# Kernel tuning notes

Hardware: AMD Instinct MI355X
Metric: run time of the kernel (lower is better)

Reference implementation:

```python
import jax, jax.numpy as jnp
import numpy as np

ALPHA = 0.1
BETA = 0.3
MARGIN = 2.0


def setup_inputs() -> dict:
    key = jax.random.key(0)
    k1, k2 = jax.random.split(key)
    prediction = jax.random.normal(k1, (8, 2048, 512), dtype=jnp.float32)
    target_seg = jax.random.randint(k2, (8, 2048), 0, 16, dtype=jnp.int64)
    return {"prediction": prediction, "target_seg": target_seg}


def _pairwise_sqdist(x):
    # x: [n, L, d] -> squared Euclidean distances [n, L, L] via a GEMM
    sq = jnp.sum(x * x, axis=-1)  # [n, L]
    inner = jnp.einsum('nld,nmd->nlm', x, x)  # [n, L, L]
    d2 = sq[:, :, None] + sq[:, None, :] - 2.0 * inner
    return jnp.maximum(d2, 0.0)


def _safe_sqrt(d2):
    # sqrt with zero (not NaN) gradient at 0, matching torch.cdist behavior
    pos = d2 > 0
    return jnp.where(pos, jnp.sqrt(jnp.where(pos, d2, 1.0)), 0.0)


def reference(prediction, target_seg):
    # y[i,j,k] = 1 if target_seg[i,j] == target_seg[i,k]
    y = (target_seg[:, :, None] == target_seg[:, None, :]).astype(prediction.dtype)
    d2 = _pairwise_sqdist(prediction)
    dist = _safe_sqrt(d2)
    hinge = jnp.maximum(MARGIN - dist, 0.0)
    loss = ALPHA * y * d2 + BETA * (1.0 - y) * hinge * hinge
    return jnp.mean(loss)
```

## Files before the change

kernel.cpp:

```cpp
#include <hip/hip_runtime.h>
#include <hip/hip_fp8.h>
#include <math.h>

#define L      2048
#define DDIM   512
#define NBATCH 8
#define NTJ    16
#define TOTAL_BLOCKS (NBATCH * NTJ * 4)

#define PANSZ  16384

#define ALPHA  0.1f
#define BETA   0.3f
#define MARGIN 2.0f

typedef __attribute__((ext_vector_type(16))) float f32x16;
typedef long long2v __attribute__((ext_vector_type(2)));

#define GLOAD_LDS16(g, l) __builtin_amdgcn_global_load_lds(              \
    (const __attribute__((address_space(1))) unsigned int*)(g),          \
    (__attribute__((address_space(3))) unsigned int*)(l), 16, 0, 0)

__global__ __launch_bounds__(256) void conv_kernel(const float* __restrict__ pred,
                                                   unsigned char* __restrict__ h,
                                                   float* __restrict__ sq) {
    int w     = threadIdx.x >> 6;
    int lane  = threadIdx.x & 63;
    int batch = blockIdx.x & 7;
    int idx   = blockIdx.x >> 3;
    int row   = batch * L + idx * 4 + w;
    const float* p = pred + (size_t)row * DDIM + lane * 8;
    float4 v0 = *(const float4*)(p);
    float4 v1 = *(const float4*)(p + 4);
    float vals[8] = {v0.x, v0.y, v0.z, v0.w, v1.x, v1.y, v1.z, v1.w};
    unsigned q[8];
    float s = 0.0f;
    #pragma unroll
    for (int i = 0; i < 8; ++i) {
        float x = vals[i];
        s = fmaf(x, x, s);
        __hip_fp8_e4m3 f8(x);
        q[i] = (unsigned)f8.__x;
    }
    unsigned lo = q[0] | (q[1] << 8) | (q[2] << 16) | (q[3] << 24);
    unsigned hi = q[4] | (q[5] << 8) | (q[6] << 16) | (q[7] << 24);
    int r5    = row & 31;
    int pair  = lane >> 2;
    int khalf = lane & 1;
    int kodd  = (lane >> 1) & 1;
    size_t off = (size_t)(row >> 5) * PANSZ + pair * 1024
               + (r5 + 32 * khalf) * 16 + kodd * 8;
    *(uint2*)(h + off) = make_uint2(lo, hi);
    #pragma unroll
    for (int o = 32; o > 0; o >>= 1) s += __shfl_down(s, o);
    if (lane == 0) sq[row] = s;
}

__global__ __launch_bounds__(256, 2) void loss_kernel(
        const unsigned char* __restrict__ h,
        const int*   __restrict__ seg,
        const float* __restrict__ sq,
        double*      __restrict__ partials) {
    __shared__ unsigned char As[65536];

    int bid = blockIdx.x;
    int n   = bid & 7;
    int r   = bid >> 3;
    int tj  = r >> 2;
    int q4  = r & 3;

    int t    = threadIdx.x;
    int wid  = t >> 6;
    int lane = t & 63;
    int wr   = wid >> 1;
    int wn   = wid & 1;
    int l31  = lane & 31;
    int hsel = lane >> 5;

    const unsigned char* base = h + (size_t)n * L * DDIM;

    {
        const unsigned char* asrc = base + (size_t)(tj * 4 + wid) * PANSZ + lane * 16;
        unsigned char* adst = As + wid * PANSZ;
        #pragma unroll
        for (int i = 0; i < 16; ++i)
            GLOAD_LDS16(asrc + i * 1024, adst + i * 1024);
    }
    __syncthreads();

    const int*   segb = seg + n * L;
    const float* sqb  = sq + n * L;

    float lsum = 0.0f;
    int aoff0 = (wr * 2 + 0) * PANSZ + lane * 16;
    int aoff1 = (wr * 2 + 1) * PANSZ + lane * 16;

    #pragma unroll 1
    for (int tkx = 0; tkx < 4; ++tkx) {
        int tk = q4 * 4 + tkx;
        const unsigned char* pb0 = base + (size_t)(tk * 4 + wn * 2) * PANSZ + lane * 16;
        const unsigned char* pb1 = pb0 + PANSZ;

        f32x16 acc[2][2];
        #pragma unroll
        for (int m = 0; m < 2; ++m)
            #pragma unroll
            for (int nf = 0; nf < 2; ++nf)
                #pragma unroll
                for (int x = 0; x < 16; ++x) acc[m][nf][x] = 0.0f;

        #pragma unroll
        for (int ks2 = 0; ks2 < 16; ++ks2) {
            long2v a0 = *(const long2v*)&As[aoff0 + ks2 * 1024];
            long2v a1 = *(const long2v*)&As[aoff1 + ks2 * 1024];
            long2v b0 = *(const long2v*)(pb0 + ks2 * 1024);
            long2v b1 = *(const long2v*)(pb1 + ks2 * 1024);
            acc[0][0] = __builtin_amdgcn_mfma_f32_32x32x16_fp8_fp8(a0.x, b0.x, acc[0][0], 0, 0, 0);
            acc[0][1] = __builtin_amdgcn_mfma_f32_32x32x16_fp8_fp8(a0.x, b1.x, acc[0][1], 0, 0, 0);
            acc[1][0] = __builtin_amdgcn_mfma_f32_32x32x16_fp8_fp8(a1.x, b0.x, acc[1][0], 0, 0, 0);
            acc[1][1] = __builtin_amdgcn_mfma_f32_32x32x16_fp8_fp8(a1.x, b1.x, acc[1][1], 0, 0, 0);
            acc[0][0] = __builtin_amdgcn_mfma_f32_32x32x16_fp8_fp8(a0.y, b0.y, acc[0][0], 0, 0, 0);
            acc[0][1] = __builtin_amdgcn_mfma_f32_32x32x16_fp8_fp8(a0.y, b1.y, acc[0][1], 0, 0, 0);
            acc[1][0] = __builtin_amdgcn_mfma_f32_32x32x16_fp8_fp8(a1.y, b0.y, acc[1][0], 0, 0, 0);
            acc[1][1] = __builtin_amdgcn_mfma_f32_32x32x16_fp8_fp8(a1.y, b1.y, acc[1][1], 0, 0, 0);
        }

        #pragma unroll
        for (int nf = 0; nf < 2; ++nf) {
            int k = tk * 128 + wn * 64 + nf * 32 + l31;
            float sqk = sqb[k];
            int   sgk = segb[k];
            #pragma unroll
            for (int m = 0; m < 2; ++m)
                #pragma unroll
                for (int x = 0; x < 16; ++x) {
                    int j = tj * 128 + wr * 64 + m * 32
                          + (x & 3) + 8 * (x >> 2) + 4 * hsel;
                    float inner = acc[m][nf][x];
                    float d2 = fmaxf(sqb[j] + sqk - 2.0f * inner, 0.0f);
                    float v;
                    if (segb[j] == sgk) {
                        v = ALPHA * d2;
                    } else {
                        float dist = sqrtf(d2);
                        float hg = fmaxf(MARGIN - dist, 0.0f);
                        v = BETA * hg * hg;
                    }
                    lsum += v;
                }
        }
    }

    double dsum = (double)lsum;
    #pragma unroll
    for (int off = 32; off > 0; off >>= 1)
        dsum += __shfl_down(dsum, off);
    if (lane == 0) partials[bid * 4 + wid] = dsum;
}

__global__ __launch_bounds__(256) void reduce_kernel(const double* __restrict__ partials,
                                                     float* __restrict__ out,
                                                     int nPart, double invCount) {
    __shared__ double red[256];
    int t = threadIdx.x;
    double s = 0.0;
    for (int i = t; i < nPart; i += 256) s += partials[i];
    red[t] = s;
    __syncthreads();
    #pragma unroll
    for (int k = 128; k > 0; k >>= 1) {
        if (t < k) red[t] += red[t + k];
        __syncthreads();
    }
    if (t == 0) out[0] = (float)(red[0] * invCount);
}

extern "C" void kernel_launch(void* const* d_in, const int* in_sizes, int n_in,
                              void* d_out, int out_size, void* d_ws, size_t ws_size,
                              hipStream_t stream) {
    const float* pred = (const float*)d_in[0];
    const int*   seg  = (const int*)d_in[1];
    float* out = (float*)d_out;

    const size_t HALF = (size_t)NBATCH * L * DDIM;
    unsigned char* h  = (unsigned char*)d_ws;
    float*  sq        = (float*)(h + HALF);
    double* partials  = (double*)(sq + NBATCH * L);

    conv_kernel<<<NBATCH * L / 4, 256, 0, stream>>>(pred, h, sq);
    loss_kernel<<<TOTAL_BLOCKS, 256, 0, stream>>>(h, seg, sq, partials);
    reduce_kernel<<<1, 256, 0, stream>>>(partials, out, TOTAL_BLOCKS * 4,
                                         1.0 / (double)((size_t)NBATCH * L * L));
}
```

Measured before the change: 66.28 us.

## Exploit distance symmetry: compute only upper-triangular tile pairs with register-prefetched operands

The distance matrix is symmetric, so the loss kernel now launches one block per upper-triangular 128x128 tile pair and weights off-diagonal entries by two. This roughly halves the GEMM and epilogue work. The LDS staging of the A panel is replaced with direct global loads through a three-deep register prefetch ring. Partial sums are reduced inside each block, so the final reduce reads fewer partials. The cost is a serial loop that decodes the triangular tile index, a per-element branch on the diagonal tiles, and B-operand reuse that now comes only from cache.

```diff
diff --git a/kernel.cpp b/kernel.cpp
--- a/kernel.cpp
+++ b/kernel.cpp
@@ -5,8 +5,11 @@
 #define L      2048
 #define DDIM   512
 #define NBATCH 8
-#define NTJ    16
-#define TOTAL_BLOCKS (NBATCH * NTJ * 4)
+#define BM     128
+#define BN     128
+#define NTILE  (L / BM)
+#define NPAIR  (NTILE * (NTILE + 1) / 2)
+#define TOTAL_BLOCKS (NBATCH * NPAIR)
 
 #define PANSZ  16384
 
@@ -16,10 +19,6 @@
 
 typedef __attribute__((ext_vector_type(16))) float f32x16;
 typedef long long2v __attribute__((ext_vector_type(2)));
-
-#define GLOAD_LDS16(g, l) __builtin_amdgcn_global_load_lds(              \
-    (const __attribute__((address_space(1))) unsigned int*)(g),          \
-    (__attribute__((address_space(3))) unsigned int*)(l), 16, 0, 0)
 
 __global__ __launch_bounds__(256) void conv_kernel(const float* __restrict__ pred,
                                                    unsigned char* __restrict__ h,
@@ -56,106 +55,117 @@
     if (lane == 0) sq[row] = s;
 }
 
-__global__ __launch_bounds__(256, 2) void loss_kernel(
+__global__ __launch_bounds__(256) void loss_kernel(
         const unsigned char* __restrict__ h,
         const int*   __restrict__ seg,
         const float* __restrict__ sq,
         double*      __restrict__ partials) {
-    __shared__ unsigned char As[65536];
+    __shared__ double wred[4];
 
     int bid = blockIdx.x;
-    int n   = bid & 7;
-    int r   = bid >> 3;
-    int tj  = r >> 2;
-    int q4  = r & 3;
+    int n = bid & 7;
+    int p = bid >> 3;
+    int tj = 0;
+    while (true) {
+        int rl2 = NTILE - tj;
+        if (p < rl2) break;
+        p -= rl2;
+        ++tj;
+    }
+    int tk = tj + p;
 
     int t    = threadIdx.x;
     int wid  = t >> 6;
     int lane = t & 63;
-    int wr   = wid >> 1;
-    int wn   = wid & 1;
+    int wr   = wid >> 1, wc = wid & 1;
     int l31  = lane & 31;
     int hsel = lane >> 5;
 
     const unsigned char* base = h + (size_t)n * L * DDIM;
 
-    {
-        const unsigned char* asrc = base + (size_t)(tj * 4 + wid) * PANSZ + lane * 16;
-        unsigned char* adst = As + wid * PANSZ;
+    const unsigned char* pa0 = base + (size_t)(tj * 4 + wr * 2 + 0) * PANSZ + lane * 16;
+    const unsigned char* pa1 = base + (size_t)(tj * 4 + wr * 2 + 1) * PANSZ + lane * 16;
+    const unsigned char* pb0 = base + (size_t)(tk * 4 + wc * 2 + 0) * PANSZ + lane * 16;
+    const unsigned char* pb1 = base + (size_t)(tk * 4 + wc * 2 + 1) * PANSZ + lane * 16;
+
+    f32x16 acc[2][2];
+    #pragma unroll
+    for (int m = 0; m < 2; ++m)
         #pragma unroll
-        for (int i = 0; i < 16; ++i)
-            GLOAD_LDS16(asrc + i * 1024, adst + i * 1024);
-    }
-    __syncthreads();
+        for (int nf = 0; nf < 2; ++nf)
+            #pragma unroll
+            for (int x = 0; x < 16; ++x) acc[m][nf][x] = 0.0f;
+
+    long2v ra0[3], ra1[3], rb0[3], rb1[3];
+    #pragma unroll
+    for (int q = 0; q < 3; ++q) {
+        ra0[q] = *(const long2v*)(pa0 + q * 1024);
+        ra1[q] = *(const long2v*)(pa1 + q * 1024);
+        rb0[q] = *(const long2v*)(pb0 + q * 1024);
+        rb1[q] = *(const long2v*)(pb1 + q * 1024);
+    }
+
+    #pragma unroll
+    for (int ks2 = 0; ks2 < 16; ++ks2) {
+        const int slot = ks2 % 3;
+        long2v a0 = ra0[slot], a1 = ra1[slot];
+        long2v b0 = rb0[slot], b1 = rb1[slot];
+
+        acc[0][0] = __builtin_amdgcn_mfma_f32_32x32x16_fp8_fp8(a0.x, b0.x, acc[0][0], 0, 0, 0);
+        acc[0][1] = __builtin_amdgcn_mfma_f32_32x32x16_fp8_fp8(a0.x, b1.x, acc[0][1], 0, 0, 0);
+        acc[1][0] = __builtin_amdgcn_mfma_f32_32x32x16_fp8_fp8(a1.x, b0.x, acc[1][0], 0, 0, 0);
+        acc[1][1] = __builtin_amdgcn_mfma_f32_32x32x16_fp8_fp8(a1.x, b1.x, acc[1][1], 0, 0, 0);
+        acc[0][0] = __builtin_amdgcn_mfma_f32_32x32x16_fp8_fp8(a0.y, b0.y, acc[0][0], 0, 0, 0);
+        acc[0][1] = __builtin_amdgcn_mfma_f32_32x32x16_fp8_fp8(a0.y, b1.y, acc[0][1], 0, 0, 0);
+        acc[1][0] = __builtin_amdgcn_mfma_f32_32x32x16_fp8_fp8(a1.y, b0.y, acc[1][0], 0, 0, 0);
+        acc[1][1] = __builtin_amdgcn_mfma_f32_32x32x16_fp8_fp8(a1.y, b1.y, acc[1][1], 0, 0, 0);
+
+        if (ks2 + 3 < 16) {
+            ra0[slot] = *(const long2v*)(pa0 + (ks2 + 3) * 1024);
+            ra1[slot] = *(const long2v*)(pa1 + (ks2 + 3) * 1024);
+            rb0[slot] = *(const long2v*)(pb0 + (ks2 + 3) * 1024);
+            rb1[slot] = *(const long2v*)(pb1 + (ks2 + 3) * 1024);
+        }
+    }
 
     const int*   segb = seg + n * L;
     const float* sqb  = sq + n * L;
+    int j0 = tj * BM, k0 = tk * BN;
 
     float lsum = 0.0f;
-    int aoff0 = (wr * 2 + 0) * PANSZ + lane * 16;
-    int aoff1 = (wr * 2 + 1) * PANSZ + lane * 16;
-
-    #pragma unroll 1
-    for (int tkx = 0; tkx < 4; ++tkx) {
-        int tk = q4 * 4 + tkx;
-        const unsigned char* pb0 = base + (size_t)(tk * 4 + wn * 2) * PANSZ + lane * 16;
-        const unsigned char* pb1 = pb0 + PANSZ;
-
-        f32x16 acc[2][2];
+    #pragma unroll
+    for (int nf = 0; nf < 2; ++nf) {
+        int k = k0 + wc * 64 + nf * 32 + l31;
+        float sqk = sqb[k];
+        int   sgk = segb[k];
         #pragma unroll
         for (int m = 0; m < 2; ++m)
             #pragma unroll
-            for (int nf = 0; nf < 2; ++nf)
-                #pragma unroll
-                for (int x = 0; x < 16; ++x) acc[m][nf][x] = 0.0f;
-
-        #pragma unroll
-        for (int ks2 = 0; ks2 < 16; ++ks2) {
-            long2v a0 = *(const long2v*)&As[aoff0 + ks2 * 1024];
-            long2v a1 = *(const long2v*)&As[aoff1 + ks2 * 1024];
-            long2v b0 = *(const long2v*)(pb0 + ks2 * 1024);
-            long2v b1 = *(const long2v*)(pb1 + ks2 * 1024);
-            acc[0][0] = __builtin_amdgcn_mfma_f32_32x32x16_fp8_fp8(a0.x, b0.x, acc[0][0], 0, 0, 0);
-            acc[0][1] = __builtin_amdgcn_mfma_f32_32x32x16_fp8_fp8(a0.x, b1.x, acc[0][1], 0, 0, 0);
-            acc[1][0] = __builtin_amdgcn_mfma_f32_32x32x16_fp8_fp8(a1.x, b0.x, acc[1][0], 0, 0, 0);
-            acc[1][1] = __builtin_amdgcn_mfma_f32_32x32x16_fp8_fp8(a1.x, b1.x, acc[1][1], 0, 0, 0);
-            acc[0][0] = __builtin_amdgcn_mfma_f32_32x32x16_fp8_fp8(a0.y, b0.y, acc[0][0], 0, 0, 0);
-            acc[0][1] = __builtin_amdgcn_mfma_f32_32x32x16_fp8_fp8(a0.y, b1.y, acc[0][1], 0, 0, 0);
-            acc[1][0] = __builtin_amdgcn_mfma_f32_32x32x16_fp8_fp8(a1.y, b0.y, acc[1][0], 0, 0, 0);
-            acc[1][1] = __builtin_amdgcn_mfma_f32_32x32x16_fp8_fp8(a1.y, b1.y, acc[1][1], 0, 0, 0);
-        }
-
-        #pragma unroll
-        for (int nf = 0; nf < 2; ++nf) {
-            int k = tk * 128 + wn * 64 + nf * 32 + l31;
-            float sqk = sqb[k];
-            int   sgk = segb[k];
-            #pragma unroll
-            for (int m = 0; m < 2; ++m)
-                #pragma unroll
-                for (int x = 0; x < 16; ++x) {
-                    int j = tj * 128 + wr * 64 + m * 32
-                          + (x & 3) + 8 * (x >> 2) + 4 * hsel;
-                    float inner = acc[m][nf][x];
-                    float d2 = fmaxf(sqb[j] + sqk - 2.0f * inner, 0.0f);
-                    float v;
-                    if (segb[j] == sgk) {
-                        v = ALPHA * d2;
-                    } else {
-                        float dist = sqrtf(d2);
-                        float hg = fmaxf(MARGIN - dist, 0.0f);
-                        v = BETA * hg * hg;
-                    }
-                    lsum += v;
+            for (int x = 0; x < 16; ++x) {
+                int j = j0 + wr * 64 + m * 32 + (x & 3) + 8 * (x >> 2) + 4 * hsel;
+                if (j > k) continue;
+                float inner = acc[m][nf][x];
+                float d2 = fmaxf(sqb[j] + sqk - 2.0f * inner, 0.0f);
+                float v;
+                if (segb[j] == sgk) {
+                    v = ALPHA * d2;
+                } else {
+                    float dist = sqrtf(d2);
+                    float hg = fmaxf(MARGIN - dist, 0.0f);
+                    v = BETA * hg * hg;
                 }
-        }
-    }
-
-    double dsum = (double)lsum;
+                lsum += (j < k) ? 2.0f * v : v;
+            }
+    }
+
+    double wgt = 1.0;
+    double dsum = (double)lsum * wgt;
     #pragma unroll
     for (int off = 32; off > 0; off >>= 1)
         dsum += __shfl_down(dsum, off);
-    if (lane == 0) partials[bid * 4 + wid] = dsum;
+    if (lane == 0) wred[wid] = dsum;
+    __syncthreads();
+    if (t == 0) partials[bid] = (wred[0] + wred[1]) + (wred[2] + wred[3]);
 }
 
 __global__ __launch_bounds__(256) void reduce_kernel(const double* __restrict__ partials,
@@ -189,6 +199,6 @@
 
     conv_kernel<<<NBATCH * L / 4, 256, 0, stream>>>(pred, h, sq);
     loss_kernel<<<TOTAL_BLOCKS, 256, 0, stream>>>(h, seg, sq, partials);
-    reduce_kernel<<<1, 256, 0, stream>>>(partials, out, TOTAL_BLOCKS * 4,
+    reduce_kernel<<<1, 256, 0, stream>>>(partials, out, TOTAL_BLOCKS,
                                          1.0 / (double)((size_t)NBATCH * L * L));
 }
```

Result: faster. 55.50 us (-16.3%).
